# Kernel optimization log

Measured on AMD Instinct MI355X. Metric: run time of the kernel, lower is better.

Reference implementation:

```python
import jax, jax.numpy as jnp
import numpy as np

N = 50000    # nodes
E = 800000   # edges per relation
R = 3        # relations
IN, HID, OUT = 128, 128, 64


def setup_inputs() -> dict:
    key = jax.random.key(0)
    ks = jax.random.split(key, 7)
    x = jax.random.normal(ks[0], (N, IN), jnp.float32)
    src = jax.random.randint(ks[1], (R, E), 0, N)
    dst = jax.random.randint(ks[2], (R, E), 0, N)
    W1 = jax.random.normal(ks[3], (R, IN, HID), jnp.float32) / np.sqrt(IN)
    b1 = jnp.zeros((R, HID), jnp.float32)
    W2 = jax.random.normal(ks[4], (R, HID, OUT), jnp.float32) / np.sqrt(HID)
    b2 = jnp.zeros((R, OUT), jnp.float32)
    return {"x": x, "src": src, "dst": dst, "W1": W1, "b1": b1, "W2": W2, "b2": b2}


def _rel_conv(x, src, dst, W, b):
    """dgl GraphConv with norm='both' and self-loops added (dgl.add_self_loop).
    out = D_dst^{-1/2} A_sl (D_src^{-1/2} X W) + b  (weight order commutes)."""
    loop = jnp.arange(N, dtype=src.dtype)
    s = jnp.concatenate([src, loop])  # [E+N] self-loops appended
    d = jnp.concatenate([dst, loop])
    ones = jnp.ones(s.shape[0], x.dtype)
    deg_out = jax.ops.segment_sum(ones, s, num_segments=N)  # >= 1 due to self loops
    deg_in = jax.ops.segment_sum(ones, d, num_segments=N)
    h = (x * jax.lax.rsqrt(deg_out)[:, None]) @ W          # [N, F_out]
    agg = jax.ops.segment_sum(h[s], d, num_segments=N)     # gather-scatter SpMM
    return agg * jax.lax.rsqrt(deg_in)[:, None] + b


def _hetero_layer(x, src, dst, W, b):
    # HeteroGraphConv with aggregate='sum': sum per-relation GraphConv outputs.
    out = _rel_conv(x, src[0], dst[0], W[0], b[0])
    for r in range(1, R):  # small fixed relation count
        out = out + _rel_conv(x, src[r], dst[r], W[r], b[r])
    return out


def reference(x, src, dst, W1, b1, W2, b2):
    h = jax.nn.relu(_hetero_layer(x, src, dst, W1, b1))
    return _hetero_layer(h, src, dst, W2, b2)
```

## Files before the change

### kernel.cpp

```cpp
#include <hip/hip_runtime.h>
#include <hip/hip_fp16.h>


constexpr int N   = 50000;
constexpr int R   = 3;
constexpr int IN  = 128;
constexpr int HID = 128;
constexpr int OUT = 64;
constexpr int M   = R * N;
constexpr int BK  = 512;
constexpr int NBKT = (M + BK - 1) / BK;
constexpr int CHUNK = 8192;
constexpr int KB  = 24;
constexpr int CVT_N4 = N * IN / 4;
constexpr int WPK   = 6 * KB * 64;
constexpr int WPK_B = (WPK + 255) / 256;

typedef _Float16 half8 __attribute__((ext_vector_type(8)));
typedef float floatx16 __attribute__((ext_vector_type(16)));

__global__ void prep_kernel(const float* __restrict__ x,
                            const float* __restrict__ W1, const float* __restrict__ W2,
                            const float* __restrict__ b1, const float* __restrict__ b2,
                            uint2* __restrict__ x16,
                            __half* __restrict__ F1, __half* __restrict__ F2,
                            float* __restrict__ bsum1, float* __restrict__ bsum2) {
    int b = blockIdx.x;
    if (b == 0) {
        int t = threadIdx.x;
        if (t < HID) bsum1[t] = b1[t] + b1[HID + t] + b1[2 * HID + t];
        if (t < OUT) bsum2[t] = b2[t] + b2[OUT + t] + b2[2 * OUT + t];
        return;
    }
    if (b <= WPK_B) {
        int idx = (b - 1) * 256 + threadIdx.x;
        if (idx < 4 * KB * 64) {
            int nt = idx / (KB * 64), rem = idx % (KB * 64);
            int kb = rem / 64, lane = rem % 64;
            int c = nt * 32 + (lane & 31);
            int k0 = kb * 16 + (lane >> 5) * 8;
            __half h[8];
#pragma unroll
            for (int j = 0; j < 8; j++) h[j] = __float2half_rn(W1[(k0 + j) * 128 + c]);
            *(uint4*)(F1 + (size_t)idx * 8) = *(uint4*)h;
        } else if (idx < 6 * KB * 64) {
            int i2 = idx - 4 * KB * 64;
            int nt = i2 / (KB * 64), rem = i2 % (KB * 64);
            int kb = rem / 64, lane = rem % 64;
            int c = nt * 32 + (lane & 31);
            int k0 = kb * 16 + (lane >> 5) * 8;
            __half h[8];
#pragma unroll
            for (int j = 0; j < 8; j++) h[j] = __float2half_rn(W2[(k0 + j) * 64 + c]);
            *(uint4*)(F2 + (size_t)i2 * 8) = *(uint4*)h;
        }
        return;
    }
    int i = (b - 1 - WPK_B) * 256 + threadIdx.x;
    if (i >= CVT_N4) return;
    float4 v = ((const float4*)x)[i];
    __half2 a = __floats2half2_rn(v.x, v.y);
    __half2 c = __floats2half2_rn(v.z, v.w);
    uint2 o;
    o.x = *(unsigned*)&a;
    o.y = *(unsigned*)&c;
    x16[i] = o;
}

__global__ __launch_bounds__(256) void p1_kernel(const int* __restrict__ src,
                                                 const int* __restrict__ dst,
                                                 int E, int RE, int nb,
                                                 int* __restrict__ bh) {
    __shared__ int hd[NBKT], hs[NBKT];
    for (int i = threadIdx.x; i < NBKT; i += 256) { hd[i] = 0; hs[i] = 0; }
    __syncthreads();
    int beg = blockIdx.x * CHUNK, end = min(RE, beg + CHUNK);
    for (int g = beg + (int)threadIdx.x; g < end; g += 256) {
        int rb = ((g >= E) + (g >= 2 * E)) * N;
        atomicAdd(&hd[(rb + dst[g]) >> 9], 1);
        atomicAdd(&hs[(rb + src[g]) >> 9], 1);
    }
    __syncthreads();
    for (int i = threadIdx.x; i < NBKT; i += 256) {
        bh[i * nb + blockIdx.x] = hd[i];
        bh[(NBKT + i) * nb + blockIdx.x] = hs[i];
    }
}

__global__ void scan1_kernel(const int* __restrict__ in, int* __restrict__ out,
                             int* __restrict__ partials, int L) {
    __shared__ int lds[1024];
    int t = threadIdx.x;
    int idx = blockIdx.x * 1024 + t;
    int v = (idx < L) ? in[idx] : 0;
    lds[t] = v;
    __syncthreads();
    for (int off = 1; off < 1024; off <<= 1) {
        int u = (t >= off) ? lds[t - off] : 0;
        __syncthreads();
        lds[t] += u;
        __syncthreads();
    }
    if (idx < L) out[idx] = lds[t] - v;
    if (t == 1023) partials[blockIdx.x] = lds[1023];
}

__global__ void scan2_kernel(int* __restrict__ partials, int nb1) {
    __shared__ int lds[256];
    int t = threadIdx.x;
    int v = (t < nb1) ? partials[t] : 0;
    lds[t] = v;
    __syncthreads();
    for (int off = 1; off < 256; off <<= 1) {
        int u = (t >= off) ? lds[t - off] : 0;
        __syncthreads();
        lds[t] += u;
        __syncthreads();
    }
    if (t < nb1) partials[t] = lds[t] - v;
}

__global__ __launch_bounds__(256) void p3_kernel(const int* __restrict__ src,
                                                 const int* __restrict__ dst,
                                                 int E, int RE, int nb,
                                                 const int* __restrict__ scanv,
                                                 const int* __restrict__ partials,
                                                 int* __restrict__ ebd,
                                                 unsigned short* __restrict__ ebs) {
    __shared__ int cd[NBKT], cs[NBKT];
    for (int i = threadIdx.x; i < NBKT; i += 256) {
        int id = i * nb + blockIdx.x;
        int is = (NBKT + i) * nb + blockIdx.x;
        cd[i] = scanv[id] + partials[id >> 10];
        cs[i] = scanv[is] + partials[is >> 10] - RE;
    }
    __syncthreads();
    int beg = blockIdx.x * CHUNK, end = min(RE, beg + CHUNK);
    for (int g = beg + (int)threadIdx.x; g < end; g += 256) {
        int rb = ((g >= E) + (g >= 2 * E)) * N;
        int s  = src[g];
        int kd = rb + dst[g];
        int pd = atomicAdd(&cd[kd >> 9], 1);
        ebd[pd] = (s << 9) | (kd & 511);
        int ks = rb + s;
        int ps = atomicAdd(&cs[ks >> 9], 1);
        ebs[ps] = (unsigned short)(ks & 511);
    }
}

__global__ __launch_bounds__(512) void pbs_kernel(const int* __restrict__ scanv,
                                                  const int* __restrict__ partials,
                                                  int nb, int RE,
                                                  const unsigned short* __restrict__ ebs,
                                                  float* __restrict__ rs_out) {
    __shared__ int cnt[BK];
    int t = threadIdx.x;
    int k = blockIdx.x;
    int i0 = (NBKT + k) * nb;
    int segbeg = scanv[i0] + partials[i0 >> 10] - RE;
    int segend;
    if (k == NBKT - 1) segend = RE;
    else {
        int i1 = i0 + nb;
        segend = scanv[i1] + partials[i1 >> 10] - RE;
    }
    cnt[t] = 0;
    __syncthreads();
    for (int e = segbeg + t; e < segend; e += 512)
        atomicAdd(&cnt[(int)ebs[e]], 1);
    __syncthreads();
    int slot = k * BK + t;
    if (slot < M) rs_out[slot] = rsqrtf((float)(cnt[t] + 1));
}

__global__ __launch_bounds__(512) void pbd_kernel(const int* __restrict__ scanv,
                                                  const int* __restrict__ partials,
                                                  int nb, int RE,
                                                  const int* __restrict__ ebd,
                                                  const float* __restrict__ rs_out,
                                                  int* __restrict__ row_ptr,
                                                  float* __restrict__ rs_in,
                                                  unsigned int* __restrict__ esrc) {
    __shared__ int cnt[BK];
    __shared__ int cur[BK];
    int t = threadIdx.x;
    int k = blockIdx.x;
    int i0 = k * nb;
    int segbeg = scanv[i0] + partials[i0 >> 10];
    int segend;
    if (k == NBKT - 1) segend = RE;
    else {
        int i1 = (k + 1) * nb;
        segend = scanv[i1] + partials[i1 >> 10];
    }
    cnt[t] = 0;
    __syncthreads();
    for (int e = segbeg + t; e < segend; e += 512)
        atomicAdd(&cnt[ebd[e] & 511], 1);
    __syncthreads();
    int slot = k * BK + t;
    int c = cnt[t];
    cur[t] = c;
    __syncthreads();
    for (int off = 1; off < 512; off <<= 1) {
        int u = (t >= off) ? cur[t - off] : 0;
        __syncthreads();
        cur[t] += u;
        __syncthreads();
    }
    int excl = cur[t] - c;
    if (slot < M) {
        row_ptr[slot] = segbeg + excl;
        rs_in[slot] = rsqrtf((float)(c + 1));
    }
    if (k == NBKT - 1 && t == 0) row_ptr[M] = RE;
    __syncthreads();
    cur[t] = segbeg + excl;
    __syncthreads();
    for (int e = segbeg + t; e < segend; e += 512) {
        int v = ebd[e];
        int key = k * BK + (v & 511);
        int r = (key >= 2 * N) + (key >= N);
        unsigned s = (unsigned)(v >> 9);
        int pos = atomicAdd(&cur[v & 511], 1);
        __half h = __float2half_rn(rs_out[r * N + s]);
        esrc[pos] = s | ((unsigned)__half_as_ushort(h) << 16);
    }
}

__global__ __launch_bounds__(256) void gather_kernel(const __half* __restrict__ Xh,
                                                     const float* __restrict__ rs_in,
                                                     const float* __restrict__ rs_out,
                                                     const int* __restrict__ row_ptr,
                                                     const unsigned int* __restrict__ esrc,
                                                     __half* __restrict__ Z16) {
    int n = blockIdx.x * 4 + (threadIdx.x >> 6);
    if (n >= N) return;
    int lane = threadIdx.x & 63;
    int pair = lane >> 5;
    int c4 = (lane & 31) * 4;
    uint2 xn = *(const uint2*)(Xh + (long)n * 128 + c4);
    const __half2 z2 = __float2half2_rn(0.f);
#pragma unroll
    for (int r = 0; r < R; r++) {
        int key = r * N + n;
        __half2 acc0 = z2, acc1 = z2;
        int beg = row_ptr[key], end = row_ptr[key + 1];
        int e = beg;
        for (; e + 16 <= end; e += 16) {
            unsigned u[8];
            uint2 y[8];
#pragma unroll
            for (int j = 0; j < 8; j++) u[j] = esrc[e + 2 * j + pair];
#pragma unroll
            for (int j = 0; j < 8; j++)
                y[j] = *(const uint2*)(Xh + (long)(u[j] & 0xffffu) * 128 + c4);
#pragma unroll
            for (int j = 0; j < 8; j++) {
                __half2 cj = __half2half2(__ushort_as_half((unsigned short)(u[j] >> 16)));
                acc0 = __hfma2(*(__half2*)&y[j].x, cj, acc0);
                acc1 = __hfma2(*(__half2*)&y[j].y, cj, acc1);
            }
        }
        for (; e + 8 <= end; e += 8) {
            unsigned u[4];
            uint2 y[4];
#pragma unroll
            for (int j = 0; j < 4; j++) u[j] = esrc[e + 2 * j + pair];
#pragma unroll
            for (int j = 0; j < 4; j++)
                y[j] = *(const uint2*)(Xh + (long)(u[j] & 0xffffu) * 128 + c4);
#pragma unroll
            for (int j = 0; j < 4; j++) {
                __half2 cj = __half2half2(__ushort_as_half((unsigned short)(u[j] >> 16)));
                acc0 = __hfma2(*(__half2*)&y[j].x, cj, acc0);
                acc1 = __hfma2(*(__half2*)&y[j].y, cj, acc1);
            }
        }
        for (; e < end; e += 2) {
            int idx = e + pair;
            unsigned u = (idx < end) ? esrc[idx] : 0u;
            uint2 y = *(const uint2*)(Xh + (long)(u & 0xffffu) * 128 + c4);
            __half2 cc = __half2half2(__ushort_as_half((unsigned short)(u >> 16)));
            acc0 = __hfma2(*(__half2*)&y.x, cc, acc0);
            acc1 = __hfma2(*(__half2*)&y.y, cc, acc1);
        }
        unsigned a0 = *(unsigned*)&acc0, a1 = *(unsigned*)&acc1;
        unsigned b0 = (unsigned)__shfl_xor((int)a0, 32, 64);
        unsigned b1 = (unsigned)__shfl_xor((int)a1, 32, 64);
        acc0 = __hadd2(acc0, *(__half2*)&b0);
        acc1 = __hadd2(acc1, *(__half2*)&b1);
        __half2 cs = __float2half2_rn(rs_out[key]);
        acc0 = __hfma2(*(__half2*)&xn.x, cs, acc0);
        acc1 = __hfma2(*(__half2*)&xn.y, cs, acc1);
        __half2 ri = __float2half2_rn(rs_in[key]);
        acc0 = __hmul2(acc0, ri);
        acc1 = __hmul2(acc1, ri);
        if (pair == 0) {
            uint2 o;
            o.x = *(unsigned*)&acc0;
            o.y = *(unsigned*)&acc1;
            *(uint2*)(Z16 + (long)n * 384 + r * 128 + c4) = o;
        }
    }
}

template <int NT, bool H16OUT>
__global__ __launch_bounds__(256) void mfma_gemm_kernel(const __half* __restrict__ Z16,
                                                        const __half* __restrict__ F,
                                                        const float* __restrict__ bias,
                                                        void* __restrict__ outp) {
    int wave = threadIdx.x >> 6, lane = threadIdx.x & 63;
    int m0 = blockIdx.x * 128 + wave * 32;
    int mrow = m0 + (lane & 31);
    int mr = min(mrow, N - 1);
    const half8* A = (const half8*)(Z16 + (long)mr * 384 + (lane >> 5) * 8);
    const half8* B = (const half8*)F;
    floatx16 acc[NT];
#pragma unroll
    for (int i = 0; i < NT; i++)
#pragma unroll
        for (int j = 0; j < 16; j++) acc[i][j] = 0.f;

    half8 a = A[0];
    for (int kb = 0; kb < KB; kb++) {
        half8 an = (kb < KB - 1) ? A[(kb + 1) * 2] : a;
#pragma unroll
        for (int nt = 0; nt < NT; nt++) {
            half8 b = B[(nt * KB + kb) * 64 + lane];
            acc[nt] = __builtin_amdgcn_mfma_f32_32x32x16_f16(a, b, acc[nt], 0, 0, 0);
        }
        a = an;
    }

    float bv[NT];
#pragma unroll
    for (int nt = 0; nt < NT; nt++) bv[nt] = bias[nt * 32 + (lane & 31)];
    int rbase = m0 + 4 * (lane >> 5);
    int col0 = lane & 31;
#pragma unroll
    for (int nt = 0; nt < NT; nt++) {
#pragma unroll
        for (int reg = 0; reg < 16; reg++) {
            int row = rbase + (reg & 3) + 8 * (reg >> 2);
            if (row < N) {
                float v = acc[nt][reg] + bv[nt];
                if (H16OUT) {
                    v = fmaxf(v, 0.f);
                    ((__half*)outp)[(long)row * (NT * 32) + nt * 32 + col0] = __float2half_rn(v);
                } else {
                    ((float*)outp)[(long)row * (NT * 32) + nt * 32 + col0] = v;
                }
            }
        }
    }
}

extern "C" void kernel_launch(void* const* d_in, const int* in_sizes, int n_in,
                              void* d_out, int out_size, void* d_ws, size_t ws_size,
                              hipStream_t stream) {
    const float* x  = (const float*)d_in[0];
    const int*  src = (const int*)d_in[1];
    const int*  dst = (const int*)d_in[2];
    const float* W1 = (const float*)d_in[3];
    const float* b1 = (const float*)d_in[4];
    const float* W2 = (const float*)d_in[5];
    const float* b2 = (const float*)d_in[6];
    float* out = (float*)d_out;
    const int E  = in_sizes[1] / R;
    const int RE = in_sizes[1];
    const int nb = (RE + CHUNK - 1) / CHUNK;
    const int L  = 2 * NBKT * nb;
    const int nb1 = (L + 1023) / 1024;

    char* ws = (char*)d_ws;
    size_t off = 0;
    auto alloc = [&](size_t bytes) -> void* {
        void* p = ws + off;
        off += (bytes + 255) & ~(size_t)255;
        return p;
    };
    float* bsum1    = (float*)alloc(HID * 4);
    float* bsum2    = (float*)alloc(OUT * 4);
    float* rs_in    = (float*)alloc((size_t)M * 4);
    float* rs_out   = (float*)alloc((size_t)M * 4);
    int*   row_ptr  = (int*)alloc((size_t)(M + 1) * 4);
    int*   bh       = (int*)alloc((size_t)L * 4);
    int*   scanv    = (int*)alloc((size_t)L * 4);
    int*   partials = (int*)alloc((size_t)nb1 * 4);
    unsigned* esrc  = (unsigned*)alloc((size_t)RE * 4);
    __half* F1      = (__half*)alloc((size_t)4 * KB * 64 * 8 * 2);
    __half* F2      = (__half*)alloc((size_t)2 * KB * 64 * 8 * 2);
    char*  regA     = (char*)alloc((size_t)N * 384 * 2);
    int*   ebd      = (int*)regA;
    unsigned short* ebs = (unsigned short*)(regA + (size_t)RE * 4);
    __half* Z16     = (__half*)regA;
    __half* x16     = (__half*)alloc((size_t)N * IN * 2);
    __half* H16     = (__half*)alloc((size_t)N * HID * 2);

    prep_kernel<<<1 + WPK_B + (CVT_N4 + 255) / 256, 256, 0, stream>>>(
        x, W1, W2, b1, b2, (uint2*)x16, F1, F2, bsum1, bsum2);
    p1_kernel<<<nb, 256, 0, stream>>>(src, dst, E, RE, nb, bh);
    scan1_kernel<<<nb1, 1024, 0, stream>>>(bh, scanv, partials, L);
    scan2_kernel<<<1, 256, 0, stream>>>(partials, nb1);
    p3_kernel<<<nb, 256, 0, stream>>>(src, dst, E, RE, nb, scanv, partials, ebd, ebs);
    pbs_kernel<<<NBKT, 512, 0, stream>>>(scanv, partials, nb, RE, ebs, rs_out);
    pbd_kernel<<<NBKT, 512, 0, stream>>>(scanv, partials, nb, RE, ebd, rs_out,
                                         row_ptr, rs_in, esrc);

    const int ab  = (N + 3) / 4;
    const int ggb = (N + 127) / 128;

    gather_kernel<<<ab, 256, 0, stream>>>(x16, rs_in, rs_out, row_ptr, esrc, Z16);
    mfma_gemm_kernel<4, true><<<ggb, 256, 0, stream>>>(Z16, F1, bsum1, H16);
    gather_kernel<<<ab, 256, 0, stream>>>(H16, rs_in, rs_out, row_ptr, esrc, Z16);
    mfma_gemm_kernel<2, false><<<ggb, 256, 0, stream>>>(Z16, F2, bsum2, out);
}
```

Baseline: 399.4 us.

## Transform before aggregating in layer two and widen bucket size to 1024

Layer two now multiplies H by each relation's W2 first, producing per-relation 64-wide fp16 outputs, and then gathers those narrower rows. This replaces the gather of 128-wide H rows into a 384-wide Z followed by a K=384 GEMM. The aim is to cut gather bandwidth and the Z16 intermediate size for the second layer, at the cost of three separate gathers over 64-wide rows and fp16 accumulation of the products. The CSR build buckets also grow from 512 to 1024 keys with 1024-thread blocks, halving the bucket count.

```diff
diff --git a/kernel.cpp b/kernel.cpp
--- a/kernel.cpp
+++ b/kernel.cpp
@@ -8,7 +8,7 @@
 constexpr int HID = 128;
 constexpr int OUT = 64;
 constexpr int M   = R * N;
-constexpr int BK  = 512;
+constexpr int BK  = 1024;
 constexpr int NBKT = (M + BK - 1) / BK;
 constexpr int CHUNK = 8192;
 constexpr int KB  = 24;
@@ -77,8 +77,8 @@
     int beg = blockIdx.x * CHUNK, end = min(RE, beg + CHUNK);
     for (int g = beg + (int)threadIdx.x; g < end; g += 256) {
         int rb = ((g >= E) + (g >= 2 * E)) * N;
-        atomicAdd(&hd[(rb + dst[g]) >> 9], 1);
-        atomicAdd(&hs[(rb + src[g]) >> 9], 1);
+        atomicAdd(&hd[(rb + dst[g]) >> 10], 1);
+        atomicAdd(&hs[(rb + src[g]) >> 10], 1);
     }
     __syncthreads();
     for (int i = threadIdx.x; i < NBKT; i += 256) {
@@ -140,19 +140,19 @@
         int rb = ((g >= E) + (g >= 2 * E)) * N;
         int s  = src[g];
         int kd = rb + dst[g];
-        int pd = atomicAdd(&cd[kd >> 9], 1);
-        ebd[pd] = (s << 9) | (kd & 511);
+        int pd = atomicAdd(&cd[kd >> 10], 1);
+        ebd[pd] = (s << 10) | (kd & 1023);
         int ks = rb + s;
-        int ps = atomicAdd(&cs[ks >> 9], 1);
-        ebs[ps] = (unsigned short)(ks & 511);
-    }
-}
-
-__global__ __launch_bounds__(512) void pbs_kernel(const int* __restrict__ scanv,
-                                                  const int* __restrict__ partials,
-                                                  int nb, int RE,
-                                                  const unsigned short* __restrict__ ebs,
-                                                  float* __restrict__ rs_out) {
+        int ps = atomicAdd(&cs[ks >> 10], 1);
+        ebs[ps] = (unsigned short)(ks & 1023);
+    }
+}
+
+__global__ __launch_bounds__(1024) void pbs_kernel(const int* __restrict__ scanv,
+                                                   const int* __restrict__ partials,
+                                                   int nb, int RE,
+                                                   const unsigned short* __restrict__ ebs,
+                                                   float* __restrict__ rs_out) {
     __shared__ int cnt[BK];
     int t = threadIdx.x;
     int k = blockIdx.x;
@@ -166,21 +166,21 @@
     }
     cnt[t] = 0;
     __syncthreads();
-    for (int e = segbeg + t; e < segend; e += 512)
+    for (int e = segbeg + t; e < segend; e += 1024)
         atomicAdd(&cnt[(int)ebs[e]], 1);
     __syncthreads();
     int slot = k * BK + t;
     if (slot < M) rs_out[slot] = rsqrtf((float)(cnt[t] + 1));
 }
 
-__global__ __launch_bounds__(512) void pbd_kernel(const int* __restrict__ scanv,
-                                                  const int* __restrict__ partials,
-                                                  int nb, int RE,
-                                                  const int* __restrict__ ebd,
-                                                  const float* __restrict__ rs_out,
-                                                  int* __restrict__ row_ptr,
-                                                  float* __restrict__ rs_in,
-                                                  unsigned int* __restrict__ esrc) {
+__global__ __launch_bounds__(1024) void pbd_kernel(const int* __restrict__ scanv,
+                                                   const int* __restrict__ partials,
+                                                   int nb, int RE,
+                                                   const int* __restrict__ ebd,
+                                                   const float* __restrict__ rs_out,
+                                                   int* __restrict__ row_ptr,
+                                                   float* __restrict__ rs_in,
+                                                   unsigned int* __restrict__ esrc) {
     __shared__ int cnt[BK];
     __shared__ int cur[BK];
     int t = threadIdx.x;
@@ -195,14 +195,14 @@
     }
     cnt[t] = 0;
     __syncthreads();
-    for (int e = segbeg + t; e < segend; e += 512)
-        atomicAdd(&cnt[ebd[e] & 511], 1);
+    for (int e = segbeg + t; e < segend; e += 1024)
+        atomicAdd(&cnt[ebd[e] & 1023], 1);
     __syncthreads();
     int slot = k * BK + t;
     int c = cnt[t];
     cur[t] = c;
     __syncthreads();
-    for (int off = 1; off < 512; off <<= 1) {
+    for (int off = 1; off < 1024; off <<= 1) {
         int u = (t >= off) ? cur[t - off] : 0;
         __syncthreads();
         cur[t] += u;
@@ -217,12 +217,12 @@
     __syncthreads();
     cur[t] = segbeg + excl;
     __syncthreads();
-    for (int e = segbeg + t; e < segend; e += 512) {
+    for (int e = segbeg + t; e < segend; e += 1024) {
         int v = ebd[e];
-        int key = k * BK + (v & 511);
+        int key = k * BK + (v & 1023);
         int r = (key >= 2 * N) + (key >= N);
-        unsigned s = (unsigned)(v >> 9);
-        int pos = atomicAdd(&cur[v & 511], 1);
+        unsigned s = (unsigned)(v >> 10);
+        int pos = atomicAdd(&cur[v & 1023], 1);
         __half h = __float2half_rn(rs_out[r * N + s]);
         esrc[pos] = s | ((unsigned)__half_as_ushort(h) << 16);
     }
@@ -305,20 +305,18 @@
     }
 }
 
-template <int NT, bool H16OUT>
-__global__ __launch_bounds__(256) void mfma_gemm_kernel(const __half* __restrict__ Z16,
-                                                        const __half* __restrict__ F,
-                                                        const float* __restrict__ bias,
-                                                        void* __restrict__ outp) {
+__global__ __launch_bounds__(256) void mfma_gemm1_kernel(const __half* __restrict__ Z16,
+                                                         const __half* __restrict__ F,
+                                                         const float* __restrict__ bias,
+                                                         __half* __restrict__ H16) {
     int wave = threadIdx.x >> 6, lane = threadIdx.x & 63;
     int m0 = blockIdx.x * 128 + wave * 32;
-    int mrow = m0 + (lane & 31);
-    int mr = min(mrow, N - 1);
+    int mr = min(m0 + (lane & 31), N - 1);
     const half8* A = (const half8*)(Z16 + (long)mr * 384 + (lane >> 5) * 8);
     const half8* B = (const half8*)F;
-    floatx16 acc[NT];
-#pragma unroll
-    for (int i = 0; i < NT; i++)
+    floatx16 acc[4];
+#pragma unroll
+    for (int i = 0; i < 4; i++)
 #pragma unroll
         for (int j = 0; j < 16; j++) acc[i][j] = 0.f;
 
@@ -326,34 +324,130 @@
     for (int kb = 0; kb < KB; kb++) {
         half8 an = (kb < KB - 1) ? A[(kb + 1) * 2] : a;
 #pragma unroll
-        for (int nt = 0; nt < NT; nt++) {
+        for (int nt = 0; nt < 4; nt++) {
             half8 b = B[(nt * KB + kb) * 64 + lane];
             acc[nt] = __builtin_amdgcn_mfma_f32_32x32x16_f16(a, b, acc[nt], 0, 0, 0);
         }
         a = an;
     }
-
-    float bv[NT];
-#pragma unroll
-    for (int nt = 0; nt < NT; nt++) bv[nt] = bias[nt * 32 + (lane & 31)];
+    float bv[4];
+#pragma unroll
+    for (int nt = 0; nt < 4; nt++) bv[nt] = bias[nt * 32 + (lane & 31)];
     int rbase = m0 + 4 * (lane >> 5);
     int col0 = lane & 31;
 #pragma unroll
-    for (int nt = 0; nt < NT; nt++) {
+    for (int nt = 0; nt < 4; nt++) {
 #pragma unroll
         for (int reg = 0; reg < 16; reg++) {
             int row = rbase + (reg & 3) + 8 * (reg >> 2);
             if (row < N) {
-                float v = acc[nt][reg] + bv[nt];
-                if (H16OUT) {
-                    v = fmaxf(v, 0.f);
-                    ((__half*)outp)[(long)row * (NT * 32) + nt * 32 + col0] = __float2half_rn(v);
-                } else {
-                    ((float*)outp)[(long)row * (NT * 32) + nt * 32 + col0] = v;
-                }
+                float v = fmaxf(acc[nt][reg] + bv[nt], 0.f);
+                H16[(long)row * 128 + nt * 32 + col0] = __float2half_rn(v);
             }
         }
     }
+}
+
+__global__ __launch_bounds__(256) void mfma_gemmY_kernel(const __half* __restrict__ H16,
+                                                         const __half* __restrict__ F,
+                                                         __half* __restrict__ Y2) {
+    int wave = threadIdx.x >> 6, lane = threadIdx.x & 63;
+    int r = blockIdx.y;
+    int m0 = blockIdx.x * 128 + wave * 32;
+    int mr = min(m0 + (lane & 31), N - 1);
+    const half8* A = (const half8*)(H16 + (long)mr * 128 + (lane >> 5) * 8);
+    const half8* B = (const half8*)F;
+    floatx16 acc[2];
+#pragma unroll
+    for (int i = 0; i < 2; i++)
+#pragma unroll
+        for (int j = 0; j < 16; j++) acc[i][j] = 0.f;
+
+#pragma unroll
+    for (int kbr = 0; kbr < 8; kbr++) {
+        half8 a = A[kbr * 2];
+#pragma unroll
+        for (int nt = 0; nt < 2; nt++) {
+            half8 b = B[(nt * KB + r * 8 + kbr) * 64 + lane];
+            acc[nt] = __builtin_amdgcn_mfma_f32_32x32x16_f16(a, b, acc[nt], 0, 0, 0);
+        }
+    }
+    int rbase = m0 + 4 * (lane >> 5);
+    int col0 = lane & 31;
+    __half* Yr = Y2 + (long)r * N * 64;
+#pragma unroll
+    for (int nt = 0; nt < 2; nt++) {
+#pragma unroll
+        for (int reg = 0; reg < 16; reg++) {
+            int row = rbase + (reg & 3) + 8 * (reg >> 2);
+            if (row < N)
+                Yr[(long)row * 64 + nt * 32 + col0] = __float2half_rn(acc[nt][reg]);
+        }
+    }
+}
+
+__global__ __launch_bounds__(256) void gather_out_kernel(const __half* __restrict__ Y2,
+                                                         const float* __restrict__ rs_in,
+                                                         const float* __restrict__ rs_out,
+                                                         const int* __restrict__ row_ptr,
+                                                         const unsigned int* __restrict__ esrc,
+                                                         const float* __restrict__ bias,
+                                                         float* __restrict__ outp) {
+    int n = blockIdx.x * 4 + (threadIdx.x >> 6);
+    if (n >= N) return;
+    int lane = threadIdx.x & 63;
+    int pair = lane >> 5;
+    int c2 = (lane & 31) * 2;
+    const __half2 z2 = __float2half2_rn(0.f);
+    float2 tot = ((const float2*)bias)[lane & 31];
+#pragma unroll
+    for (int r = 0; r < R; r++) {
+        int key = r * N + n;
+        const __half* Yr = Y2 + (long)r * N * 64;
+        __half2 acc = z2;
+        int beg = row_ptr[key], end = row_ptr[key + 1];
+        int e = beg;
+        for (; e + 16 <= end; e += 16) {
+            unsigned u[8];
+            __half2 y[8];
+#pragma unroll
+            for (int j = 0; j < 8; j++) u[j] = esrc[e + 2 * j + pair];
+#pragma unroll
+            for (int j = 0; j < 8; j++)
+                y[j] = *(const __half2*)(Yr + (long)(u[j] & 0xffffu) * 64 + c2);
+#pragma unroll
+            for (int j = 0; j < 8; j++)
+                acc = __hfma2(y[j], __half2half2(__ushort_as_half((unsigned short)(u[j] >> 16))), acc);
+        }
+        for (; e + 8 <= end; e += 8) {
+            unsigned u[4];
+            __half2 y[4];
+#pragma unroll
+            for (int j = 0; j < 4; j++) u[j] = esrc[e + 2 * j + pair];
+#pragma unroll
+            for (int j = 0; j < 4; j++)
+                y[j] = *(const __half2*)(Yr + (long)(u[j] & 0xffffu) * 64 + c2);
+#pragma unroll
+            for (int j = 0; j < 4; j++)
+                acc = __hfma2(y[j], __half2half2(__ushort_as_half((unsigned short)(u[j] >> 16))), acc);
+        }
+        for (; e < end; e += 2) {
+            int idx = e + pair;
+            unsigned u = (idx < end) ? esrc[idx] : 0u;
+            __half2 y = *(const __half2*)(Yr + (long)(u & 0xffffu) * 64 + c2);
+            acc = __hfma2(y, __half2half2(__ushort_as_half((unsigned short)(u >> 16))), acc);
+        }
+        unsigned a0 = *(unsigned*)&acc;
+        unsigned b0 = (unsigned)__shfl_xor((int)a0, 32, 64);
+        acc = __hadd2(acc, *(__half2*)&b0);
+        __half2 ys = *(const __half2*)(Yr + (long)n * 64 + c2);
+        acc = __hfma2(ys, __float2half2_rn(rs_out[key]), acc);
+        float2 f = __half22float2(acc);
+        float ri = rs_in[key];
+        tot.x += ri * f.x;
+        tot.y += ri * f.y;
+    }
+    if (pair == 0) *(float2*)(outp + (long)n * 64 + c2) = tot;
 }
 
 extern "C" void kernel_launch(void* const* d_in, const int* in_sizes, int n_in,
@@ -395,6 +489,7 @@
     int*   ebd      = (int*)regA;
     unsigned short* ebs = (unsigned short*)(regA + (size_t)RE * 4);
     __half* Z16     = (__half*)regA;
+    __half* Y2      = (__half*)regA;
     __half* x16     = (__half*)alloc((size_t)N * IN * 2);
     __half* H16     = (__half*)alloc((size_t)N * HID * 2);
 
@@ -404,15 +499,16 @@
     scan1_kernel<<<nb1, 1024, 0, stream>>>(bh, scanv, partials, L);
     scan2_kernel<<<1, 256, 0, stream>>>(partials, nb1);
     p3_kernel<<<nb, 256, 0, stream>>>(src, dst, E, RE, nb, scanv, partials, ebd, ebs);
-    pbs_kernel<<<NBKT, 512, 0, stream>>>(scanv, partials, nb, RE, ebs, rs_out);
-    pbd_kernel<<<NBKT, 512, 0, stream>>>(scanv, partials, nb, RE, ebd, rs_out,
-                                         row_ptr, rs_in, esrc);
+    pbs_kernel<<<NBKT, 1024, 0, stream>>>(scanv, partials, nb, RE, ebs, rs_out);
+    pbd_kernel<<<NBKT, 1024, 0, stream>>>(scanv, partials, nb, RE, ebd, rs_out,
+                                          row_ptr, rs_in, esrc);
 
     const int ab  = (N + 3) / 4;
     const int ggb = (N + 127) / 128;
 
     gather_kernel<<<ab, 256, 0, stream>>>(x16, rs_in, rs_out, row_ptr, esrc, Z16);
-    mfma_gemm_kernel<4, true><<<ggb, 256, 0, stream>>>(Z16, F1, bsum1, H16);
-    gather_kernel<<<ab, 256, 0, stream>>>(H16, rs_in, rs_out, row_ptr, esrc, Z16);
-    mfma_gemm_kernel<2, false><<<ggb, 256, 0, stream>>>(Z16, F2, bsum2, out);
-}
+    mfma_gemm1_kernel<<<ggb, 256, 0, stream>>>(Z16, F1, bsum1, H16);
+    mfma_gemmY_kernel<<<dim3(ggb, R), 256, 0, stream>>>(H16, F2, Y2);
+    gather_out_kernel<<<ab, 256, 0, stream>>>(Y2, rs_in, rs_out, row_ptr, esrc,
+                                              bsum2, out);
+}
```

New measurement: 364.0 us. 1.1x faster.
